# Kernel optimization log

Measured on AMD Instinct MI355X. Metric: run time of the kernel, lower is better.

Reference implementation:

```python
import jax, jax.numpy as jnp
import numpy as np

PUPIL = 256          # pupil / OPD grid size
OUTPUT_DIM = 64      # cropped PSF postage-stamp size
N_BINS = 8           # number of SED wavelength bins
BATCH = 16
# Static, wavelength-dependent diffraction padding sizes (phase_N per bin).
# In the original these come from packed_SED_data[:,0,:] but are constant in a FoV.
PHASE_NS = [1024, 988, 952, 918, 886, 856, 828, 802]


def setup_inputs() -> dict:
    key = jax.random.key(0)
    k1, k2, k3 = jax.random.split(key, 3)
    # OPD in meters: small wavefront errors (~lambda/10 rms)
    opd_batch = jax.random.normal(k1, (BATCH, PUPIL, PUPIL), dtype=jnp.float32) * 1e-7
    # Annular pupil: outer aperture with central obscuration (like Euclid/VIS optics)
    yy, xx = np.mgrid[:PUPIL, :PUPIL].astype(np.float32)
    c = (PUPIL - 1) / 2.0
    r = np.sqrt((xx - c) ** 2 + (yy - c) ** 2) / (PUPIL / 2.0)
    obscurations = jnp.asarray(((r <= 1.0) & (r >= 0.3)).astype(np.float32))
    # Observed wavelengths per bin, in meters (visible band)
    lambdas = jnp.linspace(0.55e-6, 0.9e-6, N_BINS).astype(jnp.float32)
    # Normalized SED weights
    sed = jax.random.uniform(k2, (N_BINS,), dtype=jnp.float32) + 0.1
    sed_norms = sed / jnp.sum(sed)
    return {
        "opd_batch": opd_batch,
        "obscurations": obscurations,
        "lambdas": lambdas,
        "sed_norms": sed_norms,
    }


def _mono_psf(opd, obsc, lam, phase_N, out_dim):
    """Batched monochromatic PSF: OPD -> phase -> padded FFT -> cropped |.|^2, unit-sum."""
    # opd: [B, p, p]; phase = exp(i * 2pi/lambda * opd) * obscurations
    pre_phase = (2.0 * jnp.pi / lam) * opd
    phase = (jnp.cos(pre_phase) + 1j * jnp.sin(pre_phase)).astype(jnp.complex64)
    phase = phase * obsc.astype(jnp.complex64)
    p = opd.shape[-1]
    pad_lo = (phase_N - p) // 2
    pad_hi = phase_N - p - pad_lo
    padded = jnp.pad(phase, ((0, 0), (pad_lo, pad_hi), (pad_lo, pad_hi)))  # [B, N, N]
    fft = jnp.fft.fftshift(jnp.fft.fft2(padded), axes=(-2, -1))
    psf = fft.real ** 2 + fft.imag ** 2  # |FFT|^2, float32
    start = phase_N // 2 - out_dim // 2
    psf = psf[:, start:start + out_dim, start:start + out_dim]  # central crop
    return psf / jnp.sum(psf, axis=(-2, -1), keepdims=True)


def reference(opd_batch, obscurations, lambdas, sed_norms):
    # Polychromatic PSF: SED-weighted sum of monochromatic PSFs over wavelength bins.
    # Loop is over the small fixed set of bins (distinct static FFT sizes);
    # each bin is fully vectorized over the batch.
    out = jnp.zeros((opd_batch.shape[0], OUTPUT_DIM, OUTPUT_DIM), dtype=jnp.float32)
    for b, phase_N in enumerate(PHASE_NS):
        out = out + sed_norms[b] * _mono_psf(
            opd_batch, obscurations, lambdas[b], phase_N, OUTPUT_DIM
        )
    return out
```

## Files before the change

### kernel.cpp

```cpp
#include <hip/hip_runtime.h>
#include <math.h>

#define PUPIL 256
#define N_BINS 8
#define BATCH 16

__constant__ int PHASE_NS_C[N_BINS] = {1024, 988, 952, 918, 886, 856, 828, 802};

typedef short bf16x8 __attribute__((ext_vector_type(8)));
typedef float f32x4  __attribute__((ext_vector_type(4)));
typedef int   i32x4  __attribute__((ext_vector_type(4)));

#define MFMA16(a, b, c) __builtin_amdgcn_mfma_f32_16x16x32_bf16((a), (b), (c), 0, 0, 0)

__device__ __forceinline__ short f2bf(float f) {
  unsigned u = __float_as_uint(f);
  u += 0x7FFFu + ((u >> 16) & 1u);
  return (short)(u >> 16);
}
__device__ __forceinline__ bf16x8 neg8(bf16x8 v) {
  i32x4 t = __builtin_bit_cast(i32x4, v);
  t ^= (int)0x80008000;
  return __builtin_bit_cast(bf16x8, t);
}


__global__ void wprep(short* __restrict__ Wr_t, short* __restrict__ Wi_t) {
  int idx = blockIdx.x * 256 + threadIdx.x;
  int n   = idx & 255;
  int k   = (idx >> 8) & 63;
  int bin = idx >> 14;
  int N = PHASE_NS_C[bin];
  int m = ((k - 32) * n) % N;
  if (m < 0) m += N;
  float ang = -6.283185307179586f * (float)m / (float)N;
  float s, c;
  __sincosf(ang, &s, &c);
  Wr_t[idx] = f2bf(c);
  Wi_t[idx] = f2bf(s);
}

__global__ __launch_bounds__(256, 2) void stage1(
    const float* __restrict__ opd, const float* __restrict__ obsc,
    const float* __restrict__ lambdas,
    const short* __restrict__ Wr_t, const short* __restrict__ Wi_t,
    short* __restrict__ Gr_t, short* __restrict__ Gi_t)
{
  const int tid = threadIdx.x;
  const int yb = blockIdx.x * 64, bin = blockIdx.y, b = blockIdx.z;
  const int bb = b * N_BINS + bin;
  const float w0 = 6.283185307179586f / lambdas[bin];

  const int wave = tid >> 6, lane = tid & 63;
  const int lr = lane & 15, lq = lane >> 4;

  const int y  = yb + wave * 16 + lr;
  const int x0 = lq * 8;

  const float* orow = opd + ((size_t)b * PUPIL + y) * PUPIL;
  const float* brow = obsc + (size_t)y * PUPIL;
  const short* wrb = Wr_t + ((size_t)bin * 64 + lr) * 256 + x0;
  const short* wib = Wi_t + ((size_t)bin * 64 + lr) * 256 + x0;

  f32x4 aR[4], aI[4];
  #pragma unroll
  for (int t = 0; t < 4; ++t) { aR[t] = (f32x4)0.0f; aI[t] = (f32x4)0.0f; }

  for (int xc = 0; xc < 8; ++xc) {
    const int xb = xc * 32;
    float od[8], ob[8];
    *(float4*)&od[0] = *(const float4*)(orow + xb + x0);
    *(float4*)&od[4] = *(const float4*)(orow + xb + x0 + 4);
    *(float4*)&ob[0] = *(const float4*)(brow + xb + x0);
    *(float4*)&ob[4] = *(const float4*)(brow + xb + x0 + 4);
    bf16x8 pr, pi;
    #pragma unroll
    for (int j = 0; j < 8; ++j) {
      float s, c;
      __sincosf(w0 * od[j], &s, &c);
      pr[j] = f2bf(c * ob[j]);
      pi[j] = f2bf(s * ob[j]);
    }
    #pragma unroll
    for (int t = 0; t < 4; ++t) {
      const bf16x8 w_r  = *(const bf16x8*)(wrb + (size_t)t * 16 * 256 + xb);
      const bf16x8 w_i  = *(const bf16x8*)(wib + (size_t)t * 16 * 256 + xb);
      const bf16x8 nw_i = neg8(w_i);
      aR[t] = MFMA16(w_r,  pr, aR[t]);
      aR[t] = MFMA16(nw_i, pi, aR[t]);
      aI[t] = MFMA16(w_r,  pi, aI[t]);
      aI[t] = MFMA16(w_i,  pr, aI[t]);
    }
  }

  #pragma unroll
  for (int t = 0; t < 4; ++t)
    #pragma unroll
    for (int r = 0; r < 4; ++r) {
      const int kv = t * 16 + lq * 4 + r;
      const size_t o = ((size_t)bb * 64 + kv) * 256 + y;
      Gr_t[o] = f2bf(aR[t][r]);
      Gi_t[o] = f2bf(aI[t][r]);
    }
}

__global__ __launch_bounds__(256, 4) void stage2(
    const short* __restrict__ Wr_t, const short* __restrict__ Wi_t,
    const short* __restrict__ Gr_t, const short* __restrict__ Gi_t,
    float* __restrict__ psf_raw, float* __restrict__ sums)
{
  const int tid = threadIdx.x;
  const int uc = blockIdx.x, bin = blockIdx.y, b = blockIdx.z;
  const int bb = b * N_BINS + bin;

  __shared__ float pvbuf[64 * 17];
  __shared__ float red[4];

  const int wave = tid >> 6, lane = tid & 63;
  const int lr = lane & 15, lq = lane >> 4;

  f32x4 hR = (f32x4)0.0f, hI = (f32x4)0.0f;

  const short* grb = Gr_t + ((size_t)bb * 64 + wave * 16 + lr) * 256 + lq * 8;
  const short* gib = Gi_t + ((size_t)bb * 64 + wave * 16 + lr) * 256 + lq * 8;
  const short* wrb = Wr_t + ((size_t)bin * 64 + uc * 16 + lr) * 256 + lq * 8;
  const short* wib = Wi_t + ((size_t)bin * 64 + uc * 16 + lr) * 256 + lq * 8;

  bf16x8 g_r = *(const bf16x8*)(grb);
  bf16x8 g_i = *(const bf16x8*)(gib);
  bf16x8 w_r = *(const bf16x8*)(wrb);
  bf16x8 w_i = *(const bf16x8*)(wib);

  for (int yc = 0; yc < 8; ++yc) {
    const bf16x8 cg_r = g_r, cg_i = g_i, cw_r = w_r, cw_i = w_i;
    if (yc < 7) {
      const int yn = (yc + 1) * 32;
      g_r = *(const bf16x8*)(grb + yn);
      g_i = *(const bf16x8*)(gib + yn);
      w_r = *(const bf16x8*)(wrb + yn);
      w_i = *(const bf16x8*)(wib + yn);
    }
    const bf16x8 ng_i = neg8(cg_i);
    hR = MFMA16(cg_r, cw_r, hR);
    hR = MFMA16(ng_i, cw_i, hR);
    hI = MFMA16(cg_r, cw_i, hI);
    hI = MFMA16(cg_i, cw_r, hI);
  }

  float pv[4], lsum = 0.f;
  #pragma unroll
  for (int r = 0; r < 4; ++r) {
    pv[r] = hR[r] * hR[r] + hI[r] * hI[r];
    lsum += pv[r];
  }
  #pragma unroll
  for (int off = 32; off > 0; off >>= 1) lsum += __shfl_down(lsum, off);
  if (lane == 0) red[wave] = lsum;

  #pragma unroll
  for (int r = 0; r < 4; ++r)
    pvbuf[(wave * 16 + lq * 4 + r) * 17 + lr] = pv[r];
  __syncthreads();

  if (tid == 0)
    sums[bb * 4 + uc] = red[0] + red[1] + red[2] + red[3];

  #pragma unroll
  for (int it = 0; it < 4; ++it) {
    const int i  = tid + it * 256;
    const int ul = i >> 6;
    const int v  = i & 63;
    psf_raw[(size_t)bb * 4096 + (uc * 16 + ul) * 64 + v] = pvbuf[v * 17 + ul];
  }
}

__global__ void combine(const float* __restrict__ psf_raw,
                        const float* __restrict__ sums,
                        const float* __restrict__ sed,
                        float* __restrict__ out) {
  __shared__ float sc[N_BINS];
  const int blk = blockIdx.x;
  const int b = blk >> 4;
  const int px = (blk & 15) * 256 + threadIdx.x;
  if (threadIdx.x < N_BINS) {
    const int bb = b * N_BINS + threadIdx.x;
    const float S = sums[bb * 4] + sums[bb * 4 + 1] + sums[bb * 4 + 2] + sums[bb * 4 + 3];
    sc[threadIdx.x] = sed[threadIdx.x] / S;
  }
  __syncthreads();
  float acc = 0.f;
  #pragma unroll
  for (int bin = 0; bin < N_BINS; ++bin)
    acc += sc[bin] * psf_raw[(size_t)(b * N_BINS + bin) * 4096 + px];
  out[b * 4096 + px] = acc;
}

extern "C" void kernel_launch(void* const* d_in, const int* in_sizes, int n_in,
                              void* d_out, int out_size, void* d_ws, size_t ws_size,
                              hipStream_t stream) {
  const float* opd     = (const float*)d_in[0];
  const float* obsc    = (const float*)d_in[1];
  const float* lambdas = (const float*)d_in[2];
  const float* sed     = (const float*)d_in[3];
  float* out = (float*)d_out;

  short* Wr_t = (short*)d_ws;
  short* Wi_t = Wr_t + (size_t)N_BINS * 64 * 256;
  short* Gr_t = Wi_t + (size_t)N_BINS * 64 * 256;
  short* Gi_t = Gr_t + (size_t)BATCH * N_BINS * 64 * 256;
  float* psf_raw = (float*)(Gi_t + (size_t)BATCH * N_BINS * 64 * 256);
  float* sums    = psf_raw + (size_t)BATCH * N_BINS * 4096;

  wprep<<<512, 256, 0, stream>>>(Wr_t, Wi_t);
  stage1<<<dim3(4, N_BINS, BATCH), 256, 0, stream>>>(opd, obsc, lambdas,
                                                     Wr_t, Wi_t, Gr_t, Gi_t);
  stage2<<<dim3(4, N_BINS, BATCH), 256, 0, stream>>>(Wr_t, Wi_t, Gr_t, Gi_t,
                                                     psf_raw, sums);
  combine<<<256, 256, 0, stream>>>(psf_raw, sums, sed, out);
}
```

Before: 102.1 us.

## Fuse both DFT stages into one kernel with LDS intermediate

Merges stage1 and stage2 into one kernel. Each block computes half of the output columns (32 frequencies) over all 256 rows, keeps the intermediate G in shared memory, then runs the second DFT. This removes the global round trip of the G intermediate and one kernel launch. In exchange, the phase and sincos work is recomputed twice (once per khalf block), and the grid shrinks to 256 blocks with larger shared-memory use.

```diff
diff --git a/kernel.cpp b/kernel.cpp
--- a/kernel.cpp
+++ b/kernel.cpp
@@ -24,6 +24,8 @@
   return __builtin_bit_cast(bf16x8, t);
 }
 
+
+#define GP 258
 
 __global__ void wprep(short* __restrict__ Wr_t, short* __restrict__ Wi_t) {
   int idx = blockIdx.x * 256 + threadIdx.x;
@@ -40,137 +42,125 @@
   Wi_t[idx] = f2bf(s);
 }
 
-__global__ __launch_bounds__(256, 2) void stage1(
+__global__ __launch_bounds__(256, 3) void fused(
     const float* __restrict__ opd, const float* __restrict__ obsc,
     const float* __restrict__ lambdas,
     const short* __restrict__ Wr_t, const short* __restrict__ Wi_t,
-    short* __restrict__ Gr_t, short* __restrict__ Gi_t)
-{
-  const int tid = threadIdx.x;
-  const int yb = blockIdx.x * 64, bin = blockIdx.y, b = blockIdx.z;
-  const int bb = b * N_BINS + bin;
-  const float w0 = 6.283185307179586f / lambdas[bin];
-
-  const int wave = tid >> 6, lane = tid & 63;
-  const int lr = lane & 15, lq = lane >> 4;
-
-  const int y  = yb + wave * 16 + lr;
-  const int x0 = lq * 8;
-
-  const float* orow = opd + ((size_t)b * PUPIL + y) * PUPIL;
-  const float* brow = obsc + (size_t)y * PUPIL;
-  const short* wrb = Wr_t + ((size_t)bin * 64 + lr) * 256 + x0;
-  const short* wib = Wi_t + ((size_t)bin * 64 + lr) * 256 + x0;
-
-  f32x4 aR[4], aI[4];
-  #pragma unroll
-  for (int t = 0; t < 4; ++t) { aR[t] = (f32x4)0.0f; aI[t] = (f32x4)0.0f; }
-
-  for (int xc = 0; xc < 8; ++xc) {
-    const int xb = xc * 32;
-    float od[8], ob[8];
-    *(float4*)&od[0] = *(const float4*)(orow + xb + x0);
-    *(float4*)&od[4] = *(const float4*)(orow + xb + x0 + 4);
-    *(float4*)&ob[0] = *(const float4*)(brow + xb + x0);
-    *(float4*)&ob[4] = *(const float4*)(brow + xb + x0 + 4);
-    bf16x8 pr, pi;
-    #pragma unroll
-    for (int j = 0; j < 8; ++j) {
-      float s, c;
-      __sincosf(w0 * od[j], &s, &c);
-      pr[j] = f2bf(c * ob[j]);
-      pi[j] = f2bf(s * ob[j]);
-    }
-    #pragma unroll
-    for (int t = 0; t < 4; ++t) {
-      const bf16x8 w_r  = *(const bf16x8*)(wrb + (size_t)t * 16 * 256 + xb);
-      const bf16x8 w_i  = *(const bf16x8*)(wib + (size_t)t * 16 * 256 + xb);
-      const bf16x8 nw_i = neg8(w_i);
-      aR[t] = MFMA16(w_r,  pr, aR[t]);
-      aR[t] = MFMA16(nw_i, pi, aR[t]);
-      aI[t] = MFMA16(w_r,  pi, aI[t]);
-      aI[t] = MFMA16(w_i,  pr, aI[t]);
-    }
-  }
-
-  #pragma unroll
-  for (int t = 0; t < 4; ++t)
-    #pragma unroll
-    for (int r = 0; r < 4; ++r) {
-      const int kv = t * 16 + lq * 4 + r;
-      const size_t o = ((size_t)bb * 64 + kv) * 256 + y;
-      Gr_t[o] = f2bf(aR[t][r]);
-      Gi_t[o] = f2bf(aI[t][r]);
-    }
-}
-
-__global__ __launch_bounds__(256, 4) void stage2(
-    const short* __restrict__ Wr_t, const short* __restrict__ Wi_t,
-    const short* __restrict__ Gr_t, const short* __restrict__ Gi_t,
     float* __restrict__ psf_raw, float* __restrict__ sums)
 {
   const int tid = threadIdx.x;
-  const int uc = blockIdx.x, bin = blockIdx.y, b = blockIdx.z;
+  const int khalf = blockIdx.x, bin = blockIdx.y, b = blockIdx.z;
   const int bb = b * N_BINS + bin;
-
-  __shared__ float pvbuf[64 * 17];
+  const float w0 = 6.283185307179586f / lambdas[bin];
+
+  __shared__ short Gr[32 * GP], Gi[32 * GP];
+  __shared__ float pvbuf[64 * 33];
   __shared__ float red[4];
 
   const int wave = tid >> 6, lane = tid & 63;
   const int lr = lane & 15, lq = lane >> 4;
 
-  f32x4 hR = (f32x4)0.0f, hI = (f32x4)0.0f;
-
-  const short* grb = Gr_t + ((size_t)bb * 64 + wave * 16 + lr) * 256 + lq * 8;
-  const short* gib = Gi_t + ((size_t)bb * 64 + wave * 16 + lr) * 256 + lq * 8;
-  const short* wrb = Wr_t + ((size_t)bin * 64 + uc * 16 + lr) * 256 + lq * 8;
-  const short* wib = Wi_t + ((size_t)bin * 64 + uc * 16 + lr) * 256 + lq * 8;
-
-  bf16x8 g_r = *(const bf16x8*)(grb);
-  bf16x8 g_i = *(const bf16x8*)(gib);
-  bf16x8 w_r = *(const bf16x8*)(wrb);
-  bf16x8 w_i = *(const bf16x8*)(wib);
+  const short* wrb = Wr_t + ((size_t)bin * 64 + khalf * 32 + lr) * 256 + lq * 8;
+  const short* wib = Wi_t + ((size_t)bin * 64 + khalf * 32 + lr) * 256 + lq * 8;
+
+  for (int p = 0; p < 4; ++p) {
+    const int slab = (wave * 4 + p) * 16;
+    const int y = slab + lr;
+    const float* orow = opd + ((size_t)b * PUPIL + y) * PUPIL;
+    const float* brow = obsc + (size_t)y * PUPIL;
+
+    f32x4 aR[2], aI[2];
+    aR[0] = (f32x4)0.0f; aR[1] = (f32x4)0.0f;
+    aI[0] = (f32x4)0.0f; aI[1] = (f32x4)0.0f;
+
+    for (int xc = 0; xc < 8; ++xc) {
+      const int xb = xc * 32;
+      float od[8], ob[8];
+      *(float4*)&od[0] = *(const float4*)(orow + xb + lq * 8);
+      *(float4*)&od[4] = *(const float4*)(orow + xb + lq * 8 + 4);
+      *(float4*)&ob[0] = *(const float4*)(brow + xb + lq * 8);
+      *(float4*)&ob[4] = *(const float4*)(brow + xb + lq * 8 + 4);
+      bf16x8 pr, pi;
+      #pragma unroll
+      for (int j = 0; j < 8; ++j) {
+        float s, c;
+        __sincosf(w0 * od[j], &s, &c);
+        pr[j] = f2bf(c * ob[j]);
+        pi[j] = f2bf(s * ob[j]);
+      }
+      #pragma unroll
+      for (int t = 0; t < 2; ++t) {
+        const bf16x8 w_r  = *(const bf16x8*)(wrb + (size_t)t * 16 * 256 + xb);
+        const bf16x8 w_i  = *(const bf16x8*)(wib + (size_t)t * 16 * 256 + xb);
+        const bf16x8 nw_i = neg8(w_i);
+        aR[t] = MFMA16(w_r,  pr, aR[t]);
+        aR[t] = MFMA16(nw_i, pi, aR[t]);
+        aI[t] = MFMA16(w_r,  pi, aI[t]);
+        aI[t] = MFMA16(w_i,  pr, aI[t]);
+      }
+    }
+    #pragma unroll
+    for (int t = 0; t < 2; ++t)
+      #pragma unroll
+      for (int r = 0; r < 4; ++r) {
+        const int kvl = t * 16 + lq * 4 + r;
+        Gr[kvl * GP + y] = f2bf(aR[t][r]);
+        Gi[kvl * GP + y] = f2bf(aI[t][r]);
+      }
+  }
+  __syncthreads();
+
+  const short* w2rb = Wr_t + ((size_t)bin * 64 + wave * 16 + lr) * 256 + lq * 8;
+  const short* w2ib = Wi_t + ((size_t)bin * 64 + wave * 16 + lr) * 256 + lq * 8;
+
+  f32x4 hR[2], hI[2];
+  hR[0] = (f32x4)0.0f; hR[1] = (f32x4)0.0f;
+  hI[0] = (f32x4)0.0f; hI[1] = (f32x4)0.0f;
 
   for (int yc = 0; yc < 8; ++yc) {
-    const bf16x8 cg_r = g_r, cg_i = g_i, cw_r = w_r, cw_i = w_i;
-    if (yc < 7) {
-      const int yn = (yc + 1) * 32;
-      g_r = *(const bf16x8*)(grb + yn);
-      g_i = *(const bf16x8*)(gib + yn);
-      w_r = *(const bf16x8*)(wrb + yn);
-      w_i = *(const bf16x8*)(wib + yn);
+    const int yb2 = yc * 32;
+    const bf16x8 w_r = *(const bf16x8*)(w2rb + yb2);
+    const bf16x8 w_i = *(const bf16x8*)(w2ib + yb2);
+    #pragma unroll
+    for (int t = 0; t < 2; ++t) {
+      const bf16x8 g_r  = *(const bf16x8*)&Gr[(t * 16 + lr) * GP + yb2 + lq * 8];
+      const bf16x8 g_i  = *(const bf16x8*)&Gi[(t * 16 + lr) * GP + yb2 + lq * 8];
+      const bf16x8 ng_i = neg8(g_i);
+      hR[t] = MFMA16(g_r,  w_r, hR[t]);
+      hR[t] = MFMA16(ng_i, w_i, hR[t]);
+      hI[t] = MFMA16(g_r,  w_i, hI[t]);
+      hI[t] = MFMA16(g_i,  w_r, hI[t]);
     }
-    const bf16x8 ng_i = neg8(cg_i);
-    hR = MFMA16(cg_r, cw_r, hR);
-    hR = MFMA16(ng_i, cw_i, hR);
-    hI = MFMA16(cg_r, cw_i, hI);
-    hI = MFMA16(cg_i, cw_r, hI);
-  }
-
-  float pv[4], lsum = 0.f;
-  #pragma unroll
-  for (int r = 0; r < 4; ++r) {
-    pv[r] = hR[r] * hR[r] + hI[r] * hI[r];
-    lsum += pv[r];
-  }
+  }
+
+  float pv[2][4], lsum = 0.f;
+  #pragma unroll
+  for (int t = 0; t < 2; ++t)
+    #pragma unroll
+    for (int r = 0; r < 4; ++r) {
+      pv[t][r] = hR[t][r] * hR[t][r] + hI[t][r] * hI[t][r];
+      lsum += pv[t][r];
+    }
   #pragma unroll
   for (int off = 32; off > 0; off >>= 1) lsum += __shfl_down(lsum, off);
   if (lane == 0) red[wave] = lsum;
 
-  #pragma unroll
-  for (int r = 0; r < 4; ++r)
-    pvbuf[(wave * 16 + lq * 4 + r) * 17 + lr] = pv[r];
+  const int u = wave * 16 + lr;
+  #pragma unroll
+  for (int t = 0; t < 2; ++t)
+    #pragma unroll
+    for (int r = 0; r < 4; ++r)
+      pvbuf[u * 33 + t * 16 + lq * 4 + r] = pv[t][r];
   __syncthreads();
 
   if (tid == 0)
-    sums[bb * 4 + uc] = red[0] + red[1] + red[2] + red[3];
-
-  #pragma unroll
-  for (int it = 0; it < 4; ++it) {
-    const int i  = tid + it * 256;
-    const int ul = i >> 6;
-    const int v  = i & 63;
-    psf_raw[(size_t)bb * 4096 + (uc * 16 + ul) * 64 + v] = pvbuf[v * 17 + ul];
+    sums[bb * 2 + khalf] = red[0] + red[1] + red[2] + red[3];
+
+  #pragma unroll
+  for (int k2 = 0; k2 < 8; ++k2) {
+    const int i = tid + k2 * 256;
+    const int uu = i >> 5, vl = i & 31;
+    psf_raw[(size_t)bb * 4096 + uu * 64 + khalf * 32 + vl] = pvbuf[uu * 33 + vl];
   }
 }
 
@@ -184,8 +174,7 @@
   const int px = (blk & 15) * 256 + threadIdx.x;
   if (threadIdx.x < N_BINS) {
     const int bb = b * N_BINS + threadIdx.x;
-    const float S = sums[bb * 4] + sums[bb * 4 + 1] + sums[bb * 4 + 2] + sums[bb * 4 + 3];
-    sc[threadIdx.x] = sed[threadIdx.x] / S;
+    sc[threadIdx.x] = sed[threadIdx.x] / (sums[bb * 2] + sums[bb * 2 + 1]);
   }
   __syncthreads();
   float acc = 0.f;
@@ -206,15 +195,11 @@
 
   short* Wr_t = (short*)d_ws;
   short* Wi_t = Wr_t + (size_t)N_BINS * 64 * 256;
-  short* Gr_t = Wi_t + (size_t)N_BINS * 64 * 256;
-  short* Gi_t = Gr_t + (size_t)BATCH * N_BINS * 64 * 256;
-  float* psf_raw = (float*)(Gi_t + (size_t)BATCH * N_BINS * 64 * 256);
+  float* psf_raw = (float*)(Wi_t + (size_t)N_BINS * 64 * 256);
   float* sums    = psf_raw + (size_t)BATCH * N_BINS * 4096;
 
   wprep<<<512, 256, 0, stream>>>(Wr_t, Wi_t);
-  stage1<<<dim3(4, N_BINS, BATCH), 256, 0, stream>>>(opd, obsc, lambdas,
-                                                     Wr_t, Wi_t, Gr_t, Gi_t);
-  stage2<<<dim3(4, N_BINS, BATCH), 256, 0, stream>>>(Wr_t, Wi_t, Gr_t, Gi_t,
-                                                     psf_raw, sums);
+  fused<<<dim3(2, N_BINS, BATCH), 256, 0, stream>>>(opd, obsc, lambdas,
+                                                    Wr_t, Wi_t, psf_raw, sums);
   combine<<<256, 256, 0, stream>>>(psf_raw, sums, sed, out);
 }
```

After: 95.74 us. -6.3%, faster.
